# Performance work log

Measured on AMD Instinct MI355X. Metric: run time of the kernel, lower is better.

Reference implementation:

```python
import jax, jax.numpy as jnp
import numpy as np


def _lstm_layer(x_seq, w_ih, w_hh, b_ih, b_hh):
    # x_seq: [T, in], PyTorch gate order i, f, g, o
    H = w_hh.shape[1]
    h0 = jnp.zeros((H,), x_seq.dtype)

    def step(carry, x_t):
        h, c = carry
        gates = x_t @ w_ih.T + h @ w_hh.T + b_ih + b_hh  # [4H]
        i, f, g, o = jnp.split(gates, 4)
        i = jax.nn.sigmoid(i)
        f = jax.nn.sigmoid(f)
        g = jnp.tanh(g)
        o = jax.nn.sigmoid(o)
        c = f * c + i * g
        h = o * jnp.tanh(c)
        return (h, c), h

    _, hs = jax.lax.scan(step, (h0, h0), x_seq)
    return hs  # [T, H]


def setup_inputs() -> dict:
    key = jax.random.key(0)
    ks = jax.random.split(key, 12)
    B, T, n, H = 8, 128, 32, 128
    s = 1.0 / np.sqrt(H)

    def u(k, shape):
        return jax.random.uniform(k, shape, jnp.float32, -s, s)

    return {
        "x": jax.random.normal(ks[0], (B, T, n, n), jnp.float32),
        "w_ih0": u(ks[1], (4 * H, 1)),
        "w_hh0": u(ks[2], (4 * H, H)),
        "b_ih0": u(ks[3], (4 * H,)),
        "b_hh0": u(ks[4], (4 * H,)),
        "w_ih1": u(ks[5], (4 * H, H)),
        "w_hh1": u(ks[6], (4 * H, H)),
        "b_ih1": u(ks[7], (4 * H,)),
        "b_hh1": u(ks[8], (4 * H,)),
        "w_out": u(ks[9], (1, H)),
        "b_out": u(ks[10], (1,)),
    }


def reference(x, w_ih0, w_hh0, b_ih0, b_hh0, w_ih1, w_hh1, b_ih1, b_hh1, w_out, b_out):
    # x: [B, T, n, n]
    def rnn_forward(xi):  # xi: [T, n, n] -> out [T, 1]
        u = jnp.trace(xi, axis1=-2, axis2=-1)[:, None]  # [T, 1]
        h1 = _lstm_layer(u, w_ih0, w_hh0, b_ih0, b_hh0)
        h2 = _lstm_layer(h1, w_ih1, w_hh1, b_ih1, b_hh1)
        return h2 @ w_out.T + b_out  # [T, 1]

    jac = jax.vmap(jax.jacrev(rnn_forward))(x)  # [B, T, 1, T, n, n]
    d = jnp.diagonal(jac, axis1=1, axis2=3)      # [B, 1, n, n, T]
    # mirror torch: [:, 0] then transpose(2,3).transpose(1,2) -> [B, T, n, n]
    return jnp.transpose(d[:, 0], (0, 3, 1, 2))
```

## Files before the change

kernel.cpp:

```cpp
#include <hip/hip_runtime.h>
#include <math.h>

#define H    128
#define TT   128
#define CH   8
#define NCH  (TT / CH)

#define OFF_H1V   0
#define OFF_PARTS 262144
#define OFF_CNT   1441792

typedef __attribute__((ext_vector_type(2))) float f2;

__device__ __forceinline__ float sigf(float x)       { return 1.0f / (1.0f + __expf(-x)); }
__device__ __forceinline__ float tanhf_fast(float x) { return 1.0f - 2.0f / (1.0f + __expf(2.0f * x)); }

__device__ __forceinline__ float quad_sum(float v) {
    int t = __builtin_amdgcn_update_dpp(0, __float_as_int(v), 0xB1, 0xF, 0xF, true);
    v += __int_as_float(t);
    t = __builtin_amdgcn_update_dpp(0, __float_as_int(v), 0x4E, 0xF, 0xF, true);
    v += __int_as_float(t);
    return v;
}

__device__ __forceinline__ void wait_ge(int* ptr, int val) {
    while (__hip_atomic_load(ptr, __ATOMIC_RELAXED, __HIP_MEMORY_SCOPE_AGENT) < val)
        __builtin_amdgcn_s_sleep(1);
    (void)__hip_atomic_load(ptr, __ATOMIC_ACQUIRE, __HIP_MEMORY_SCOPE_AGENT);
}

#define BARRIER_LGKM() do { \
    asm volatile("s_waitcnt lgkmcnt(0)" ::: "memory"); \
    __builtin_amdgcn_s_barrier(); \
    asm volatile("" ::: "memory"); \
} while (0)

#define BARRIER_ALL() do { \
    asm volatile("s_waitcnt vmcnt(0) lgkmcnt(0)" ::: "memory"); \
    __builtin_amdgcn_s_barrier(); \
    asm volatile("" ::: "memory"); \
} while (0)

#define DECLW4(nm, src) \
    float4 _t_##nm = (src); \
    f2 nm##_a = {_t_##nm.x, _t_##nm.y}; \
    f2 nm##_b = {_t_##nm.z, _t_##nm.w}; \
    asm volatile("" : "+v"(nm##_a), "+v"(nm##_b));

#define LOADW_ALL(W) \
    const float4* wpa_ = (const float4*)((W) + (size_t)(rg)       * H + p * 32); \
    const float4* wpb_ = (const float4*)((W) + (size_t)(rg + 128) * H + p * 32); \
    const float4* wpc_ = (const float4*)((W) + (size_t)(rg + 256) * H + p * 32); \
    const float4* wpd_ = (const float4*)((W) + (size_t)(rg + 384) * H + p * 32); \
    DECLW4(wa0, wpa_[0]) DECLW4(wa1, wpa_[1]) DECLW4(wa2, wpa_[2]) DECLW4(wa3, wpa_[3]) \
    DECLW4(wa4, wpa_[4]) DECLW4(wa5, wpa_[5]) DECLW4(wa6, wpa_[6]) DECLW4(wa7, wpa_[7]) \
    DECLW4(wb0, wpb_[0]) DECLW4(wb1, wpb_[1]) DECLW4(wb2, wpb_[2]) DECLW4(wb3, wpb_[3]) \
    DECLW4(wb4, wpb_[4]) DECLW4(wb5, wpb_[5]) DECLW4(wb6, wpb_[6]) DECLW4(wb7, wpb_[7]) \
    DECLW4(wc0, wpc_[0]) DECLW4(wc1, wpc_[1]) DECLW4(wc2, wpc_[2]) DECLW4(wc3, wpc_[3]) \
    DECLW4(wc4, wpc_[4]) DECLW4(wc5, wpc_[5]) DECLW4(wc6, wpc_[6]) DECLW4(wc7, wpc_[7]) \
    DECLW4(wd0, wpd_[0]) DECLW4(wd1, wpd_[1]) DECLW4(wd2, wpd_[2]) DECLW4(wd3, wpd_[3]) \
    DECLW4(wd4, wpd_[4]) DECLW4(wd5, wpd_[5]) DECLW4(wd6, wpd_[6]) DECLW4(wd7, wpd_[7])

#define PKFMA(acc, w, h) \
    asm("v_pk_fma_f32 %0, %1, %2, %0" : "+v"(acc) : "v"(w), "v"(h));

#define FMA1(nm, hA, hB, acc) PKFMA(acc, nm##_a, hA) PKFMA(acc, nm##_b, hB)

#define DOTJ(j) { \
    f2 hA_ = {hv##j.x, hv##j.y}; f2 hB_ = {hv##j.z, hv##j.w}; \
    FMA1(wa##j, hA_, hB_, q0) FMA1(wb##j, hA_, hB_, q1) \
    FMA1(wc##j, hA_, hB_, q2) FMA1(wd##j, hA_, hB_, q3) }

#define DOT_BODY(HBASE) \
    const float4* _hp4 = (const float4*)(HBASE); \
    float4 hv0=_hp4[0],hv1=_hp4[1],hv2=_hp4[2],hv3=_hp4[3], \
           hv4=_hp4[4],hv5=_hp4[5],hv6=_hp4[6],hv7=_hp4[7]; \
    f2 q0={0.f,0.f},q1={0.f,0.f},q2={0.f,0.f},q3={0.f,0.f}; \
    DOTJ(0) DOTJ(1) DOTJ(2) DOTJ(3) DOTJ(4) DOTJ(5) DOTJ(6) DOTJ(7) \
    float a0=q0.x+q0.y, a1=q1.x+q1.y, a2=q2.x+q2.y, a3=q3.x+q3.y; \
    a0 = quad_sum(a0); a1 = quad_sum(a1); a2 = quad_sum(a2); a3 = quad_sum(a3);

__global__ __launch_bounds__(512)
__attribute__((amdgpu_waves_per_eu(1, 2)))
void pipe_kernel(const float* __restrict__ x,
                 const float* __restrict__ w_ih0,
                 const float* __restrict__ w_hh0,
                 const float* __restrict__ b_ih0,
                 const float* __restrict__ b_hh0,
                 const float* __restrict__ w_ih1,
                 const float* __restrict__ w_hh1,
                 const float* __restrict__ b_ih1,
                 const float* __restrict__ b_hh1,
                 const float* __restrict__ w_out,
                 float* __restrict__ ws,
                 float* __restrict__ outp) {
    const int role = blockIdx.x >> 3;
    const int b    = blockIdx.x & 7;
    const int r    = threadIdx.x;
    const int rg   = r >> 2, p = r & 3;
    const int wsl  = rg >> 5, wpos = rg & 31;

    int* cntA  = (int*)ws + OFF_CNT       + b * 32;
    int* cntB1 = (int*)ws + OFF_CNT + 256 + b * 32;
    int* cntB2 = (int*)ws + OFF_CNT + 512 + b * 32;
    float* h1v = ws + OFF_H1V + (size_t)b * TT * 256;

    __shared__ float hbuf[2][144];
    __shared__ float u_s[TT];
    __shared__ float scr[512];
    __shared__ float hb[CH * 144];
    __shared__ float gbuf[CH][128];

    if (role == 0) {
        LOADW_ALL(w_hh0)
        const float b0 = b_ih0[rg]       + b_hh0[rg];
        const float b1 = b_ih0[rg + 128] + b_hh0[rg + 128];
        const float b2 = b_ih0[rg + 256] + b_hh0[rg + 256];
        const float b3 = b_ih0[rg + 384] + b_hh0[rg + 384];
        const float wi0 = w_ih0[rg], wi1 = w_ih0[rg + 128];
        const float wi2 = w_ih0[rg + 256], wi3 = w_ih0[rg + 384];
        {
            const float* xb = x + (size_t)(b * TT + (r & 127)) * 1024;
            const int pq = r >> 7;
            float u = 0.f;
#pragma unroll
            for (int i = 0; i < 8; i++) u += xb[(pq * 8 + i) * 33];
            scr[r] = u;
        }
        if (r < 144) hbuf[0][r] = 0.f;
        __syncthreads();
        if (r < TT) u_s[r] = scr[r] + scr[r + 128] + scr[r + 256] + scr[r + 384];
        __syncthreads();

        float c1 = 0.f;
        float hn_prev = 0.f, vn_prev = 0.f;
        for (int t = 0; t < TT; t++) {
            if (t & (CH - 1)) {
                if (p == 0) h1v[(t - 1) * 256 + rg] = hn_prev;
                if (p == 1) h1v[(t - 1) * 256 + 128 + rg] = vn_prev;
            }
            const float u = u_s[t];
            const float* hc = hbuf[t & 1];
            float* hx = hbuf[(t & 1) ^ 1];
            DOT_BODY(hc + p * 36)
            float z0 = a0 + fmaf(wi0, u, b0);
            float z1 = a1 + fmaf(wi1, u, b1);
            float z2 = a2 + fmaf(wi2, u, b2);
            float z3 = a3 + fmaf(wi3, u, b3);
            float gi = sigf(z0), gf = sigf(z1), gg = tanhf_fast(z2), go = sigf(z3);
            float di = gi * (1.f - gi) * wi0, df = gf * (1.f - gf) * wi1;
            float dg = (1.f - gg * gg) * wi2, dd = go * (1.f - go) * wi3;
            float dc = df * c1 + di * gg + gi * dg;
            c1 = gf * c1 + gi * gg;
            float th = tanhf_fast(c1);
            float hn = go * th;
            float vn = dd * th + go * (1.f - th * th) * dc;
            if (p == wsl) hx[p * 36 + wpos] = hn;
            if ((t & (CH - 1)) == CH - 1) {
                if (p == 0) h1v[t * 256 + rg] = hn;
                if (p == 1) h1v[t * 256 + 128 + rg] = vn;
                BARRIER_ALL();
                if (r == 0)
                    __hip_atomic_store(cntA, t + 1, __ATOMIC_RELEASE, __HIP_MEMORY_SCOPE_AGENT);
            } else {
                hn_prev = hn; vn_prev = vn;
                BARRIER_LGKM();
            }
        }
    } else if (role == 1 || role == 2) {
        LOADW_ALL(w_ih1)
        int* myCnt = (role == 2) ? cntB2 : cntB1;
        const float* hsrc = h1v + ((role == 2) ? 128 : 0);
        float* pbase = ws + OFF_PARTS + (size_t)b * TT * 1024 + ((role == 2) ? 512 : 0);
        for (int c = 0; c < NCH; c++) {
            if (r == 0) wait_ge(cntA, (c + 1) * CH);
            __syncthreads();
            if (r < 256) {
                int tl = r >> 5, k4 = r & 31, s = k4 >> 3, j = k4 & 7;
                float4 v = *(const float4*)(hsrc + (size_t)(c * CH + tl) * 256 + k4 * 4);
                *(float4*)&hb[(tl * 4 + s) * 36 + j * 4] = v;
            }
            __syncthreads();
#pragma unroll
            for (int tl = 0; tl < CH; tl++) {
                DOT_BODY(hb + (tl * 4 + p) * 36)
                float sel = (p == 0) ? a0 : (p == 1) ? a1 : (p == 2) ? a2 : a3;
                pbase[(size_t)(c * CH + tl) * 1024 + r] = sel;
            }
            BARRIER_ALL();
            if (r == 0)
                __hip_atomic_store(myCnt, (c + 1) * CH, __ATOMIC_RELEASE, __HIP_MEMORY_SCOPE_AGENT);
        }
    } else {
        LOADW_ALL(w_hh1)
        const float b0 = b_ih1[rg]       + b_hh1[rg];
        const float b1 = b_ih1[rg + 128] + b_hh1[rg + 128];
        const float b2 = b_ih1[rg + 256] + b_hh1[rg + 256];
        const float b3 = b_ih1[rg + 384] + b_hh1[rg + 384];
        const float wo = w_out[rg];
        if (r < 144) hbuf[0][r] = 0.f;
        __syncthreads();
        const float* parts = ws + OFF_PARTS + (size_t)b * TT * 1024;
        float c2 = 0.f;
        for (int c = 0; c < NCH; c++) {
            if (r == 0) { wait_ge(cntB1, (c + 1) * CH); wait_ge(cntB2, (c + 1) * CH); }
            __syncthreads();
            float4 zf[CH], af[CH];
#pragma unroll
            for (int tl = 0; tl < CH; tl++) {
                zf[tl] = *(const float4*)(parts + (size_t)(c * CH + tl) * 1024 + rg * 4);
                af[tl] = *(const float4*)(parts + (size_t)(c * CH + tl) * 1024 + 512 + rg * 4);
            }
#pragma unroll
            for (int tl = 0; tl < CH; tl++) {
                const int t = c * CH + tl;
                const float* hc = hbuf[t & 1];
                float* hx = hbuf[(t & 1) ^ 1];
                DOT_BODY(hc + p * 36)
                float z0 = a0 + b0 + zf[tl].x;
                float z1 = a1 + b1 + zf[tl].y;
                float z2 = a2 + b2 + zf[tl].z;
                float z3 = a3 + b3 + zf[tl].w;
                float gi = sigf(z0), gf = sigf(z1), gg = tanhf_fast(z2), go = sigf(z3);
                float di = gi * (1.f - gi) * af[tl].x, df = gf * (1.f - gf) * af[tl].y;
                float dg = (1.f - gg * gg) * af[tl].z, dd = go * (1.f - go) * af[tl].w;
                float dc = df * c2 + di * gg + gi * dg;
                c2 = gf * c2 + gi * gg;
                float th = tanhf_fast(c2);
                if (p == wsl) hx[p * 36 + wpos] = go * th;
                float dh2 = dd * th + go * (1.f - th * th) * dc;
                if (p == 0) gbuf[tl][rg] = wo * dh2;
                BARRIER_LGKM();
            }
            {
                const int w = r >> 6, l = r & 63;
                float v = gbuf[w][l] + gbuf[w][l + 64];
                v = quad_sum(v);
                v += __shfl_xor(v, 4, 64);
                v += __shfl_xor(v, 8, 64);
                v += __shfl_xor(v, 16, 64);
                v += __shfl_xor(v, 32, 64);
                if (l == 0) scr[w] = v;
                BARRIER_LGKM();
                if (r < 256) {
                    const int tl = r >> 5, d = r & 31;
                    outp[(size_t)(b * TT + c * CH + tl) * 1024 + d * 33] = scr[tl];
                }
            }
        }
    }
}

extern "C" void kernel_launch(void* const* d_in, const int* in_sizes, int n_in,
                              void* d_out, int out_size, void* d_ws, size_t ws_size,
                              hipStream_t stream) {
    const float* x     = (const float*)d_in[0];
    const float* w_ih0 = (const float*)d_in[1];
    const float* w_hh0 = (const float*)d_in[2];
    const float* b_ih0 = (const float*)d_in[3];
    const float* b_hh0 = (const float*)d_in[4];
    const float* w_ih1 = (const float*)d_in[5];
    const float* w_hh1 = (const float*)d_in[6];
    const float* b_ih1 = (const float*)d_in[7];
    const float* b_hh1 = (const float*)d_in[8];
    const float* w_out = (const float*)d_in[9];

    float* ws = (float*)d_ws;

    hipMemsetAsync(d_out, 0, (size_t)out_size, stream);

    pipe_kernel<<<dim3(32), dim3(512), 0, stream>>>(x, w_ih0, w_hh0, b_ih0, b_hh0,
                                                    w_ih1, w_hh1, b_ih1, b_hh1, w_out,
                                                    ws, (float*)d_out);
}
```

Before: 235.1 us.

## Halve block size to 256 threads with two lanes per gate row

Each block now uses 256 threads, and two lanes share a gate row with 64 weights each held in registers, instead of four lanes with 32 each. This cuts the cross-lane reduction from a quad sum to a pair sum and drops the padded LDS layout. The intent is fewer waves to synchronise per recurrent step and a shorter reduction chain. In exchange each lane runs twice as many FMAs per step and holds twice as many weight registers, which lengthens the serial per-step work.

```diff
diff --git a/kernel.cpp b/kernel.cpp
--- a/kernel.cpp
+++ b/kernel.cpp
@@ -15,6 +15,10 @@
 __device__ __forceinline__ float sigf(float x)       { return 1.0f / (1.0f + __expf(-x)); }
 __device__ __forceinline__ float tanhf_fast(float x) { return 1.0f - 2.0f / (1.0f + __expf(2.0f * x)); }
 
+__device__ __forceinline__ float pair_sum(float v) {
+    int t = __builtin_amdgcn_update_dpp(0, __float_as_int(v), 0xB1, 0xF, 0xF, true);
+    return v + __int_as_float(t);
+}
 __device__ __forceinline__ float quad_sum(float v) {
     int t = __builtin_amdgcn_update_dpp(0, __float_as_int(v), 0xB1, 0xF, 0xF, true);
     v += __int_as_float(t);
@@ -47,19 +51,18 @@
     f2 nm##_b = {_t_##nm.z, _t_##nm.w}; \
     asm volatile("" : "+v"(nm##_a), "+v"(nm##_b));
 
+#define DECLG(g, ptr) \
+    DECLW4(g##0,(ptr)[0])  DECLW4(g##1,(ptr)[1])  DECLW4(g##2,(ptr)[2])  DECLW4(g##3,(ptr)[3]) \
+    DECLW4(g##4,(ptr)[4])  DECLW4(g##5,(ptr)[5])  DECLW4(g##6,(ptr)[6])  DECLW4(g##7,(ptr)[7]) \
+    DECLW4(g##8,(ptr)[8])  DECLW4(g##9,(ptr)[9])  DECLW4(g##10,(ptr)[10]) DECLW4(g##11,(ptr)[11]) \
+    DECLW4(g##12,(ptr)[12]) DECLW4(g##13,(ptr)[13]) DECLW4(g##14,(ptr)[14]) DECLW4(g##15,(ptr)[15])
+
 #define LOADW_ALL(W) \
-    const float4* wpa_ = (const float4*)((W) + (size_t)(rg)       * H + p * 32); \
-    const float4* wpb_ = (const float4*)((W) + (size_t)(rg + 128) * H + p * 32); \
-    const float4* wpc_ = (const float4*)((W) + (size_t)(rg + 256) * H + p * 32); \
-    const float4* wpd_ = (const float4*)((W) + (size_t)(rg + 384) * H + p * 32); \
-    DECLW4(wa0, wpa_[0]) DECLW4(wa1, wpa_[1]) DECLW4(wa2, wpa_[2]) DECLW4(wa3, wpa_[3]) \
-    DECLW4(wa4, wpa_[4]) DECLW4(wa5, wpa_[5]) DECLW4(wa6, wpa_[6]) DECLW4(wa7, wpa_[7]) \
-    DECLW4(wb0, wpb_[0]) DECLW4(wb1, wpb_[1]) DECLW4(wb2, wpb_[2]) DECLW4(wb3, wpb_[3]) \
-    DECLW4(wb4, wpb_[4]) DECLW4(wb5, wpb_[5]) DECLW4(wb6, wpb_[6]) DECLW4(wb7, wpb_[7]) \
-    DECLW4(wc0, wpc_[0]) DECLW4(wc1, wpc_[1]) DECLW4(wc2, wpc_[2]) DECLW4(wc3, wpc_[3]) \
-    DECLW4(wc4, wpc_[4]) DECLW4(wc5, wpc_[5]) DECLW4(wc6, wpc_[6]) DECLW4(wc7, wpc_[7]) \
-    DECLW4(wd0, wpd_[0]) DECLW4(wd1, wpd_[1]) DECLW4(wd2, wpd_[2]) DECLW4(wd3, wpd_[3]) \
-    DECLW4(wd4, wpd_[4]) DECLW4(wd5, wpd_[5]) DECLW4(wd6, wpd_[6]) DECLW4(wd7, wpd_[7])
+    const float4* wpa_ = (const float4*)((W) + (size_t)(rg)       * H + p * 64); \
+    const float4* wpb_ = (const float4*)((W) + (size_t)(rg + 128) * H + p * 64); \
+    const float4* wpc_ = (const float4*)((W) + (size_t)(rg + 256) * H + p * 64); \
+    const float4* wpd_ = (const float4*)((W) + (size_t)(rg + 384) * H + p * 64); \
+    DECLG(wa, wpa_) DECLG(wb, wpb_) DECLG(wc, wpc_) DECLG(wd, wpd_)
 
 #define PKFMA(acc, w, h) \
     asm("v_pk_fma_f32 %0, %1, %2, %0" : "+v"(acc) : "v"(w), "v"(h));
@@ -74,14 +77,16 @@
 #define DOT_BODY(HBASE) \
     const float4* _hp4 = (const float4*)(HBASE); \
     float4 hv0=_hp4[0],hv1=_hp4[1],hv2=_hp4[2],hv3=_hp4[3], \
-           hv4=_hp4[4],hv5=_hp4[5],hv6=_hp4[6],hv7=_hp4[7]; \
+           hv4=_hp4[4],hv5=_hp4[5],hv6=_hp4[6],hv7=_hp4[7], \
+           hv8=_hp4[8],hv9=_hp4[9],hv10=_hp4[10],hv11=_hp4[11], \
+           hv12=_hp4[12],hv13=_hp4[13],hv14=_hp4[14],hv15=_hp4[15]; \
     f2 q0={0.f,0.f},q1={0.f,0.f},q2={0.f,0.f},q3={0.f,0.f}; \
     DOTJ(0) DOTJ(1) DOTJ(2) DOTJ(3) DOTJ(4) DOTJ(5) DOTJ(6) DOTJ(7) \
-    float a0=q0.x+q0.y, a1=q1.x+q1.y, a2=q2.x+q2.y, a3=q3.x+q3.y; \
-    a0 = quad_sum(a0); a1 = quad_sum(a1); a2 = quad_sum(a2); a3 = quad_sum(a3);
-
-__global__ __launch_bounds__(512)
-__attribute__((amdgpu_waves_per_eu(1, 2)))
+    DOTJ(8) DOTJ(9) DOTJ(10) DOTJ(11) DOTJ(12) DOTJ(13) DOTJ(14) DOTJ(15) \
+    float a0=pair_sum(q0.x+q0.y), a1=pair_sum(q1.x+q1.y), \
+          a2=pair_sum(q2.x+q2.y), a3=pair_sum(q3.x+q3.y);
+
+__global__ __launch_bounds__(256, 1)
 void pipe_kernel(const float* __restrict__ x,
                  const float* __restrict__ w_ih0,
                  const float* __restrict__ w_hh0,
@@ -97,18 +102,17 @@
     const int role = blockIdx.x >> 3;
     const int b    = blockIdx.x & 7;
     const int r    = threadIdx.x;
-    const int rg   = r >> 2, p = r & 3;
-    const int wsl  = rg >> 5, wpos = rg & 31;
+    const int rg   = r >> 1, p = r & 1;
 
     int* cntA  = (int*)ws + OFF_CNT       + b * 32;
     int* cntB1 = (int*)ws + OFF_CNT + 256 + b * 32;
     int* cntB2 = (int*)ws + OFF_CNT + 512 + b * 32;
     float* h1v = ws + OFF_H1V + (size_t)b * TT * 256;
 
-    __shared__ float hbuf[2][144];
+    __shared__ float hbuf[2][128];
     __shared__ float u_s[TT];
-    __shared__ float scr[512];
-    __shared__ float hb[CH * 144];
+    __shared__ float scr[256];
+    __shared__ float hb[CH * 128];
     __shared__ float gbuf[CH][128];
 
     if (role == 0) {
@@ -124,12 +128,12 @@
             const int pq = r >> 7;
             float u = 0.f;
 #pragma unroll
-            for (int i = 0; i < 8; i++) u += xb[(pq * 8 + i) * 33];
+            for (int i = 0; i < 16; i++) u += xb[(pq * 16 + i) * 33];
             scr[r] = u;
         }
-        if (r < 144) hbuf[0][r] = 0.f;
+        if (r < 128) { hbuf[0][r] = 0.f; hbuf[1][r] = 0.f; }
         __syncthreads();
-        if (r < TT) u_s[r] = scr[r] + scr[r + 128] + scr[r + 256] + scr[r + 384];
+        if (r < TT) u_s[r] = scr[r] + scr[r + 128];
         __syncthreads();
 
         float c1 = 0.f;
@@ -137,12 +141,12 @@
         for (int t = 0; t < TT; t++) {
             if (t & (CH - 1)) {
                 if (p == 0) h1v[(t - 1) * 256 + rg] = hn_prev;
-                if (p == 1) h1v[(t - 1) * 256 + 128 + rg] = vn_prev;
+                else        h1v[(t - 1) * 256 + 128 + rg] = vn_prev;
             }
             const float u = u_s[t];
             const float* hc = hbuf[t & 1];
-            float* hx = hbuf[(t & 1) ^ 1];
-            DOT_BODY(hc + p * 36)
+            float* hx = (float*)hbuf[(t & 1) ^ 1];
+            DOT_BODY(hc + p * 64)
             float z0 = a0 + fmaf(wi0, u, b0);
             float z1 = a1 + fmaf(wi1, u, b1);
             float z2 = a2 + fmaf(wi2, u, b2);
@@ -155,10 +159,10 @@
             float th = tanhf_fast(c1);
             float hn = go * th;
             float vn = dd * th + go * (1.f - th * th) * dc;
-            if (p == wsl) hx[p * 36 + wpos] = hn;
+            if (p == 0) hx[rg] = hn;
             if ((t & (CH - 1)) == CH - 1) {
                 if (p == 0) h1v[t * 256 + rg] = hn;
-                if (p == 1) h1v[t * 256 + 128 + rg] = vn;
+                else        h1v[t * 256 + 128 + rg] = vn;
                 BARRIER_ALL();
                 if (r == 0)
                     __hip_atomic_store(cntA, t + 1, __ATOMIC_RELEASE, __HIP_MEMORY_SCOPE_AGENT);
@@ -175,17 +179,18 @@
         for (int c = 0; c < NCH; c++) {
             if (r == 0) wait_ge(cntA, (c + 1) * CH);
             __syncthreads();
-            if (r < 256) {
-                int tl = r >> 5, k4 = r & 31, s = k4 >> 3, j = k4 & 7;
+            {
+                int tl = r >> 5, k4 = r & 31;
                 float4 v = *(const float4*)(hsrc + (size_t)(c * CH + tl) * 256 + k4 * 4);
-                *(float4*)&hb[(tl * 4 + s) * 36 + j * 4] = v;
+                *(float4*)&hb[tl * 128 + k4 * 4] = v;
             }
             __syncthreads();
 #pragma unroll
             for (int tl = 0; tl < CH; tl++) {
-                DOT_BODY(hb + (tl * 4 + p) * 36)
-                float sel = (p == 0) ? a0 : (p == 1) ? a1 : (p == 2) ? a2 : a3;
-                pbase[(size_t)(c * CH + tl) * 1024 + r] = sel;
+                DOT_BODY(hb + tl * 128 + p * 64)
+                f2 st;
+                if (p == 0) { st.x = a0; st.y = a1; } else { st.x = a2; st.y = a3; }
+                *(f2*)(pbase + (size_t)(c * CH + tl) * 1024 + rg * 4 + p * 2) = st;
             }
             BARRIER_ALL();
             if (r == 0)
@@ -198,51 +203,52 @@
         const float b2 = b_ih1[rg + 256] + b_hh1[rg + 256];
         const float b3 = b_ih1[rg + 384] + b_hh1[rg + 384];
         const float wo = w_out[rg];
-        if (r < 144) hbuf[0][r] = 0.f;
+        if (r < 128) { hbuf[0][r] = 0.f; hbuf[1][r] = 0.f; }
         __syncthreads();
         const float* parts = ws + OFF_PARTS + (size_t)b * TT * 1024;
         float c2 = 0.f;
         for (int c = 0; c < NCH; c++) {
             if (r == 0) { wait_ge(cntB1, (c + 1) * CH); wait_ge(cntB2, (c + 1) * CH); }
             __syncthreads();
-            float4 zf[CH], af[CH];
-#pragma unroll
-            for (int tl = 0; tl < CH; tl++) {
-                zf[tl] = *(const float4*)(parts + (size_t)(c * CH + tl) * 1024 + rg * 4);
-                af[tl] = *(const float4*)(parts + (size_t)(c * CH + tl) * 1024 + 512 + rg * 4);
-            }
 #pragma unroll
             for (int tl = 0; tl < CH; tl++) {
                 const int t = c * CH + tl;
+                const float* pt = parts + (size_t)t * 1024 + rg * 4;
+                float4 zf = *(const float4*)pt;
+                float4 af = *(const float4*)(pt + 512);
                 const float* hc = hbuf[t & 1];
-                float* hx = hbuf[(t & 1) ^ 1];
-                DOT_BODY(hc + p * 36)
-                float z0 = a0 + b0 + zf[tl].x;
-                float z1 = a1 + b1 + zf[tl].y;
-                float z2 = a2 + b2 + zf[tl].z;
-                float z3 = a3 + b3 + zf[tl].w;
+                float* hx = (float*)hbuf[(t & 1) ^ 1];
+                DOT_BODY(hc + p * 64)
+                float z0 = a0 + b0 + zf.x;
+                float z1 = a1 + b1 + zf.y;
+                float z2 = a2 + b2 + zf.z;
+                float z3 = a3 + b3 + zf.w;
                 float gi = sigf(z0), gf = sigf(z1), gg = tanhf_fast(z2), go = sigf(z3);
-                float di = gi * (1.f - gi) * af[tl].x, df = gf * (1.f - gf) * af[tl].y;
-                float dg = (1.f - gg * gg) * af[tl].z, dd = go * (1.f - go) * af[tl].w;
+                float di = gi * (1.f - gi) * af.x, df = gf * (1.f - gf) * af.y;
+                float dg = (1.f - gg * gg) * af.z, dd = go * (1.f - go) * af.w;
                 float dc = df * c2 + di * gg + gi * dg;
                 c2 = gf * c2 + gi * gg;
                 float th = tanhf_fast(c2);
-                if (p == wsl) hx[p * 36 + wpos] = go * th;
+                if (p == 0) hx[rg] = go * th;
                 float dh2 = dd * th + go * (1.f - th * th) * dc;
                 if (p == 0) gbuf[tl][rg] = wo * dh2;
                 BARRIER_LGKM();
             }
             {
                 const int w = r >> 6, l = r & 63;
-                float v = gbuf[w][l] + gbuf[w][l + 64];
-                v = quad_sum(v);
-                v += __shfl_xor(v, 4, 64);
-                v += __shfl_xor(v, 8, 64);
-                v += __shfl_xor(v, 16, 64);
-                v += __shfl_xor(v, 32, 64);
-                if (l == 0) scr[w] = v;
+#pragma unroll
+                for (int tt = 0; tt < 2; tt++) {
+                    const int t8 = w * 2 + tt;
+                    float v = gbuf[t8][l] + gbuf[t8][l + 64];
+                    v = quad_sum(v);
+                    v += __shfl_xor(v, 4, 64);
+                    v += __shfl_xor(v, 8, 64);
+                    v += __shfl_xor(v, 16, 64);
+                    v += __shfl_xor(v, 32, 64);
+                    if (l == 0) scr[t8] = v;
+                }
                 BARRIER_LGKM();
-                if (r < 256) {
+                {
                     const int tl = r >> 5, d = r & 31;
                     outp[(size_t)(b * TT + c * CH + tl) * 1024 + d * 33] = scr[tl];
                 }
@@ -269,7 +275,7 @@
 
     hipMemsetAsync(d_out, 0, (size_t)out_size, stream);
 
-    pipe_kernel<<<dim3(32), dim3(512), 0, stream>>>(x, w_ih0, w_hh0, b_ih0, b_hh0,
+    pipe_kernel<<<dim3(32), dim3(256), 0, stream>>>(x, w_ih0, w_hh0, b_ih0, b_hh0,
                                                     w_ih1, w_hh1, b_ih1, b_hh1, w_out,
                                                     ws, (float*)d_out);
 }
```

Result: slower. 357.6 us (+52.1%).

## Split pipelined persistent kernel into three sequential kernels without spin-wait flags

Applied to the files above, without the earlier changes.

Replaces the single 32-block persistent kernel, whose role blocks handed data to each other through atomic counters and spin waits, with three launches: layer-1 recurrence, a parallel input projection over 128 blocks, and the layer-2 recurrence. This removes the cross-block polling and release/acquire overhead and lets the projection run fully in parallel. In exchange it gives up the overlap between layer 1 and layer 2, so the two serial recurrences now run back to back, and it adds launch overhead.

```diff
diff --git a/kernel.cpp b/kernel.cpp
--- a/kernel.cpp
+++ b/kernel.cpp
@@ -8,7 +8,6 @@
 
 #define OFF_H1V   0
 #define OFF_PARTS 262144
-#define OFF_CNT   1441792
 
 typedef __attribute__((ext_vector_type(2))) float f2;
 
@@ -23,20 +22,8 @@
     return v;
 }
 
-__device__ __forceinline__ void wait_ge(int* ptr, int val) {
-    while (__hip_atomic_load(ptr, __ATOMIC_RELAXED, __HIP_MEMORY_SCOPE_AGENT) < val)
-        __builtin_amdgcn_s_sleep(1);
-    (void)__hip_atomic_load(ptr, __ATOMIC_ACQUIRE, __HIP_MEMORY_SCOPE_AGENT);
-}
-
 #define BARRIER_LGKM() do { \
     asm volatile("s_waitcnt lgkmcnt(0)" ::: "memory"); \
-    __builtin_amdgcn_s_barrier(); \
-    asm volatile("" ::: "memory"); \
-} while (0)
-
-#define BARRIER_ALL() do { \
-    asm volatile("s_waitcnt vmcnt(0) lgkmcnt(0)" ::: "memory"); \
     __builtin_amdgcn_s_barrier(); \
     asm volatile("" ::: "memory"); \
 } while (0)
@@ -82,170 +69,170 @@
 
 __global__ __launch_bounds__(512)
 __attribute__((amdgpu_waves_per_eu(1, 2)))
-void pipe_kernel(const float* __restrict__ x,
-                 const float* __restrict__ w_ih0,
-                 const float* __restrict__ w_hh0,
-                 const float* __restrict__ b_ih0,
-                 const float* __restrict__ b_hh0,
-                 const float* __restrict__ w_ih1,
-                 const float* __restrict__ w_hh1,
-                 const float* __restrict__ b_ih1,
-                 const float* __restrict__ b_hh1,
-                 const float* __restrict__ w_out,
-                 float* __restrict__ ws,
-                 float* __restrict__ outp) {
-    const int role = blockIdx.x >> 3;
-    const int b    = blockIdx.x & 7;
-    const int r    = threadIdx.x;
-    const int rg   = r >> 2, p = r & 3;
-    const int wsl  = rg >> 5, wpos = rg & 31;
-
-    int* cntA  = (int*)ws + OFF_CNT       + b * 32;
-    int* cntB1 = (int*)ws + OFF_CNT + 256 + b * 32;
-    int* cntB2 = (int*)ws + OFF_CNT + 512 + b * 32;
+void k1_layer1(const float* __restrict__ x,
+               const float* __restrict__ w_ih0,
+               const float* __restrict__ w_hh0,
+               const float* __restrict__ b_ih0,
+               const float* __restrict__ b_hh0,
+               float* __restrict__ ws) {
+    const int b  = blockIdx.x;
+    const int r  = threadIdx.x;
+    const int rg = r >> 2, p = r & 3;
+    const int wsl = rg >> 5, wpos = rg & 31;
     float* h1v = ws + OFF_H1V + (size_t)b * TT * 256;
 
     __shared__ float hbuf[2][144];
     __shared__ float u_s[TT];
     __shared__ float scr[512];
-    __shared__ float hb[CH * 144];
+
+    LOADW_ALL(w_hh0)
+    const float b0 = b_ih0[rg]       + b_hh0[rg];
+    const float b1 = b_ih0[rg + 128] + b_hh0[rg + 128];
+    const float b2 = b_ih0[rg + 256] + b_hh0[rg + 256];
+    const float b3 = b_ih0[rg + 384] + b_hh0[rg + 384];
+    const float wi0 = w_ih0[rg], wi1 = w_ih0[rg + 128];
+    const float wi2 = w_ih0[rg + 256], wi3 = w_ih0[rg + 384];
+    {
+        const float* xb = x + (size_t)(b * TT + (r & 127)) * 1024;
+        const int pq = r >> 7;
+        float u = 0.f;
+#pragma unroll
+        for (int i = 0; i < 8; i++) u += xb[(pq * 8 + i) * 33];
+        scr[r] = u;
+    }
+    if (r < 144) hbuf[0][r] = 0.f;
+    __syncthreads();
+    if (r < TT) u_s[r] = scr[r] + scr[r + 128] + scr[r + 256] + scr[r + 384];
+    __syncthreads();
+
+    float c1 = 0.f;
+    for (int t = 0; t < TT; t++) {
+        const float u = u_s[t];
+        const float* hc = hbuf[t & 1];
+        float* hx = hbuf[(t & 1) ^ 1];
+        DOT_BODY(hc + p * 36)
+        float z0 = a0 + fmaf(wi0, u, b0);
+        float z1 = a1 + fmaf(wi1, u, b1);
+        float z2 = a2 + fmaf(wi2, u, b2);
+        float z3 = a3 + fmaf(wi3, u, b3);
+        float gi = sigf(z0), gf = sigf(z1), gg = tanhf_fast(z2), go = sigf(z3);
+        float di = gi * (1.f - gi) * wi0, df = gf * (1.f - gf) * wi1;
+        float dg = (1.f - gg * gg) * wi2, dd = go * (1.f - go) * wi3;
+        float dc = df * c1 + di * gg + gi * dg;
+        c1 = gf * c1 + gi * gg;
+        float th = tanhf_fast(c1);
+        float hn = go * th;
+        float vn = dd * th + go * (1.f - th * th) * dc;
+        if (p == wsl) hx[p * 36 + wpos] = hn;
+        if (p == 0) h1v[t * 256 + rg] = hn;
+        if (p == 1) h1v[t * 256 + 128 + rg] = vn;
+        BARRIER_LGKM();
+    }
+}
+
+__global__ __launch_bounds__(512)
+void k2_proj(const float* __restrict__ w_ih1, float* __restrict__ ws) {
+    const int c = blockIdx.x & 15;
+    const int b = blockIdx.x >> 4;
+    const int r = threadIdx.x;
+    const int rg = r >> 2, p = r & 3;
+    const float* h1v = ws + OFF_H1V + (size_t)b * TT * 256;
+    float* pbase = ws + OFF_PARTS + (size_t)b * TT * 1024;
+
+    __shared__ float hbA[CH * 144];
+    __shared__ float hbB[CH * 144];
+
+    LOADW_ALL(w_ih1)
+    {
+        const int rr = r & 255;
+        const int tl = rr >> 5, k4 = rr & 31, s = k4 >> 3, j = k4 & 7;
+        const float* src = h1v + (size_t)(c * CH + tl) * 256 + ((r < 256) ? 0 : 128);
+        float4 v = *(const float4*)(src + k4 * 4);
+        float* dst = (r < 256) ? hbA : hbB;
+        *(float4*)&dst[(tl * 4 + s) * 36 + j * 4] = v;
+    }
+    __syncthreads();
+#pragma unroll
+    for (int tl = 0; tl < CH; tl++) {
+        {
+            DOT_BODY(hbA + (tl * 4 + p) * 36)
+            float sel = (p == 0) ? a0 : (p == 1) ? a1 : (p == 2) ? a2 : a3;
+            pbase[(size_t)(c * CH + tl) * 1024 + r] = sel;
+        }
+        {
+            DOT_BODY(hbB + (tl * 4 + p) * 36)
+            float sel = (p == 0) ? a0 : (p == 1) ? a1 : (p == 2) ? a2 : a3;
+            pbase[(size_t)(c * CH + tl) * 1024 + 512 + r] = sel;
+        }
+    }
+}
+
+__global__ __launch_bounds__(512)
+__attribute__((amdgpu_waves_per_eu(1, 2)))
+void k3_layer2(const float* __restrict__ w_hh1,
+               const float* __restrict__ b_ih1,
+               const float* __restrict__ b_hh1,
+               const float* __restrict__ w_out,
+               const float* __restrict__ ws,
+               float* __restrict__ outp) {
+    const int b  = blockIdx.x;
+    const int r  = threadIdx.x;
+    const int rg = r >> 2, p = r & 3;
+    const int wsl = rg >> 5, wpos = rg & 31;
+    const float* parts = ws + OFF_PARTS + (size_t)b * TT * 1024;
+
+    __shared__ float hbuf[2][144];
+    __shared__ float scr[512];
     __shared__ float gbuf[CH][128];
 
-    if (role == 0) {
-        LOADW_ALL(w_hh0)
-        const float b0 = b_ih0[rg]       + b_hh0[rg];
-        const float b1 = b_ih0[rg + 128] + b_hh0[rg + 128];
-        const float b2 = b_ih0[rg + 256] + b_hh0[rg + 256];
-        const float b3 = b_ih0[rg + 384] + b_hh0[rg + 384];
-        const float wi0 = w_ih0[rg], wi1 = w_ih0[rg + 128];
-        const float wi2 = w_ih0[rg + 256], wi3 = w_ih0[rg + 384];
-        {
-            const float* xb = x + (size_t)(b * TT + (r & 127)) * 1024;
-            const int pq = r >> 7;
-            float u = 0.f;
+    LOADW_ALL(w_hh1)
+    const float b0 = b_ih1[rg]       + b_hh1[rg];
+    const float b1 = b_ih1[rg + 128] + b_hh1[rg + 128];
+    const float b2 = b_ih1[rg + 256] + b_hh1[rg + 256];
+    const float b3 = b_ih1[rg + 384] + b_hh1[rg + 384];
+    const float wo = w_out[rg];
+    if (r < 144) hbuf[0][r] = 0.f;
+    __syncthreads();
+
+    float c2 = 0.f;
+    for (int c = 0; c < NCH; c++) {
 #pragma unroll
-            for (int i = 0; i < 8; i++) u += xb[(pq * 8 + i) * 33];
-            scr[r] = u;
-        }
-        if (r < 144) hbuf[0][r] = 0.f;
-        __syncthreads();
-        if (r < TT) u_s[r] = scr[r] + scr[r + 128] + scr[r + 256] + scr[r + 384];
-        __syncthreads();
-
-        float c1 = 0.f;
-        float hn_prev = 0.f, vn_prev = 0.f;
-        for (int t = 0; t < TT; t++) {
-            if (t & (CH - 1)) {
-                if (p == 0) h1v[(t - 1) * 256 + rg] = hn_prev;
-                if (p == 1) h1v[(t - 1) * 256 + 128 + rg] = vn_prev;
-            }
-            const float u = u_s[t];
+        for (int tl = 0; tl < CH; tl++) {
+            const int t = c * CH + tl;
+            const float* pt = parts + (size_t)t * 1024 + rg * 4;
+            float4 zf = *(const float4*)pt;
+            float4 af = *(const float4*)(pt + 512);
             const float* hc = hbuf[t & 1];
             float* hx = hbuf[(t & 1) ^ 1];
             DOT_BODY(hc + p * 36)
-            float z0 = a0 + fmaf(wi0, u, b0);
-            float z1 = a1 + fmaf(wi1, u, b1);
-            float z2 = a2 + fmaf(wi2, u, b2);
-            float z3 = a3 + fmaf(wi3, u, b3);
+            float z0 = a0 + b0 + zf.x;
+            float z1 = a1 + b1 + zf.y;
+            float z2 = a2 + b2 + zf.z;
+            float z3 = a3 + b3 + zf.w;
             float gi = sigf(z0), gf = sigf(z1), gg = tanhf_fast(z2), go = sigf(z3);
-            float di = gi * (1.f - gi) * wi0, df = gf * (1.f - gf) * wi1;
-            float dg = (1.f - gg * gg) * wi2, dd = go * (1.f - go) * wi3;
-            float dc = df * c1 + di * gg + gi * dg;
-            c1 = gf * c1 + gi * gg;
-            float th = tanhf_fast(c1);
-            float hn = go * th;
-            float vn = dd * th + go * (1.f - th * th) * dc;
-            if (p == wsl) hx[p * 36 + wpos] = hn;
-            if ((t & (CH - 1)) == CH - 1) {
-                if (p == 0) h1v[t * 256 + rg] = hn;
-                if (p == 1) h1v[t * 256 + 128 + rg] = vn;
-                BARRIER_ALL();
-                if (r == 0)
-                    __hip_atomic_store(cntA, t + 1, __ATOMIC_RELEASE, __HIP_MEMORY_SCOPE_AGENT);
-            } else {
-                hn_prev = hn; vn_prev = vn;
-                BARRIER_LGKM();
-            }
-        }
-    } else if (role == 1 || role == 2) {
-        LOADW_ALL(w_ih1)
-        int* myCnt = (role == 2) ? cntB2 : cntB1;
-        const float* hsrc = h1v + ((role == 2) ? 128 : 0);
-        float* pbase = ws + OFF_PARTS + (size_t)b * TT * 1024 + ((role == 2) ? 512 : 0);
-        for (int c = 0; c < NCH; c++) {
-            if (r == 0) wait_ge(cntA, (c + 1) * CH);
-            __syncthreads();
+            float di = gi * (1.f - gi) * af.x, df = gf * (1.f - gf) * af.y;
+            float dg = (1.f - gg * gg) * af.z, dd = go * (1.f - go) * af.w;
+            float dc = df * c2 + di * gg + gi * dg;
+            c2 = gf * c2 + gi * gg;
+            float th = tanhf_fast(c2);
+            if (p == wsl) hx[p * 36 + wpos] = go * th;
+            float dh2 = dd * th + go * (1.f - th * th) * dc;
+            if (p == 0) gbuf[tl][rg] = wo * dh2;
+            BARRIER_LGKM();
+        }
+        {
+            const int w = r >> 6, l = r & 63;
+            float v = gbuf[w][l] + gbuf[w][l + 64];
+            v = quad_sum(v);
+            v += __shfl_xor(v, 4, 64);
+            v += __shfl_xor(v, 8, 64);
+            v += __shfl_xor(v, 16, 64);
+            v += __shfl_xor(v, 32, 64);
+            if (l == 0) scr[w] = v;
+            BARRIER_LGKM();
             if (r < 256) {
-                int tl = r >> 5, k4 = r & 31, s = k4 >> 3, j = k4 & 7;
-                float4 v = *(const float4*)(hsrc + (size_t)(c * CH + tl) * 256 + k4 * 4);
-                *(float4*)&hb[(tl * 4 + s) * 36 + j * 4] = v;
-            }
-            __syncthreads();
-#pragma unroll
-            for (int tl = 0; tl < CH; tl++) {
-                DOT_BODY(hb + (tl * 4 + p) * 36)
-                float sel = (p == 0) ? a0 : (p == 1) ? a1 : (p == 2) ? a2 : a3;
-                pbase[(size_t)(c * CH + tl) * 1024 + r] = sel;
-            }
-            BARRIER_ALL();
-            if (r == 0)
-                __hip_atomic_store(myCnt, (c + 1) * CH, __ATOMIC_RELEASE, __HIP_MEMORY_SCOPE_AGENT);
-        }
-    } else {
-        LOADW_ALL(w_hh1)
-        const float b0 = b_ih1[rg]       + b_hh1[rg];
-        const float b1 = b_ih1[rg + 128] + b_hh1[rg + 128];
-        const float b2 = b_ih1[rg + 256] + b_hh1[rg + 256];
-        const float b3 = b_ih1[rg + 384] + b_hh1[rg + 384];
-        const float wo = w_out[rg];
-        if (r < 144) hbuf[0][r] = 0.f;
-        __syncthreads();
-        const float* parts = ws + OFF_PARTS + (size_t)b * TT * 1024;
-        float c2 = 0.f;
-        for (int c = 0; c < NCH; c++) {
-            if (r == 0) { wait_ge(cntB1, (c + 1) * CH); wait_ge(cntB2, (c + 1) * CH); }
-            __syncthreads();
-            float4 zf[CH], af[CH];
-#pragma unroll
-            for (int tl = 0; tl < CH; tl++) {
-                zf[tl] = *(const float4*)(parts + (size_t)(c * CH + tl) * 1024 + rg * 4);
-                af[tl] = *(const float4*)(parts + (size_t)(c * CH + tl) * 1024 + 512 + rg * 4);
-            }
-#pragma unroll
-            for (int tl = 0; tl < CH; tl++) {
-                const int t = c * CH + tl;
-                const float* hc = hbuf[t & 1];
-                float* hx = hbuf[(t & 1) ^ 1];
-                DOT_BODY(hc + p * 36)
-                float z0 = a0 + b0 + zf[tl].x;
-                float z1 = a1 + b1 + zf[tl].y;
-                float z2 = a2 + b2 + zf[tl].z;
-                float z3 = a3 + b3 + zf[tl].w;
-                float gi = sigf(z0), gf = sigf(z1), gg = tanhf_fast(z2), go = sigf(z3);
-                float di = gi * (1.f - gi) * af[tl].x, df = gf * (1.f - gf) * af[tl].y;
-                float dg = (1.f - gg * gg) * af[tl].z, dd = go * (1.f - go) * af[tl].w;
-                float dc = df * c2 + di * gg + gi * dg;
-                c2 = gf * c2 + gi * gg;
-                float th = tanhf_fast(c2);
-                if (p == wsl) hx[p * 36 + wpos] = go * th;
-                float dh2 = dd * th + go * (1.f - th * th) * dc;
-                if (p == 0) gbuf[tl][rg] = wo * dh2;
-                BARRIER_LGKM();
-            }
-            {
-                const int w = r >> 6, l = r & 63;
-                float v = gbuf[w][l] + gbuf[w][l + 64];
-                v = quad_sum(v);
-                v += __shfl_xor(v, 4, 64);
-                v += __shfl_xor(v, 8, 64);
-                v += __shfl_xor(v, 16, 64);
-                v += __shfl_xor(v, 32, 64);
-                if (l == 0) scr[w] = v;
-                BARRIER_LGKM();
-                if (r < 256) {
-                    const int tl = r >> 5, d = r & 31;
-                    outp[(size_t)(b * TT + c * CH + tl) * 1024 + d * 33] = scr[tl];
-                }
+                const int tl = r >> 5, d = r & 31;
+                outp[(size_t)(b * TT + c * CH + tl) * 1024 + d * 33] = scr[tl];
             }
         }
     }
@@ -269,7 +256,8 @@
 
     hipMemsetAsync(d_out, 0, (size_t)out_size, stream);
 
-    pipe_kernel<<<dim3(32), dim3(512), 0, stream>>>(x, w_ih0, w_hh0, b_ih0, b_hh0,
-                                                    w_ih1, w_hh1, b_ih1, b_hh1, w_out,
-                                                    ws, (float*)d_out);
-}
+    k1_layer1<<<dim3(8),   dim3(512), 0, stream>>>(x, w_ih0, w_hh0, b_ih0, b_hh0, ws);
+    k2_proj  <<<dim3(128), dim3(512), 0, stream>>>(w_ih1, ws);
+    k3_layer2<<<dim3(8),   dim3(512), 0, stream>>>(w_hh1, b_ih1, b_hh1, w_out, ws,
+                                                   (float*)d_out);
+}
```

New measurement: 367.8 us. 56.4% more time.
